# Optimization experiments

Hardware: AMD Instinct MI355X
Metric: run time of the kernel (lower is better)

The kernel has to match this reference:

```python
import jax, jax.numpy as jnp
import numpy as np

NU, NI = 32768, 8192
N = NU + NI
DIM = 64
E = 2_000_000
KNN_K = 10
N_LAYERS = 2
MM_LAYERS = 1
MM_IMG_W = 0.1
THRESHOLD = 0.0


def _knn_adj(feat, k=KNN_K):
    # mirrors get_knn_adj_mat + compute_normalized_laplacian (built on frozen feats)
    fn = feat / np.linalg.norm(feat, axis=1, keepdims=True)
    sim = fn @ fn.T                              # [NI, NI]
    knn = np.argpartition(-sim, k, axis=1)[:, :k]
    rows = np.repeat(np.arange(feat.shape[0]), k)
    cols = knn.reshape(-1)
    deg = np.bincount(rows, minlength=feat.shape[0]).astype(np.float32) + 1e-7
    rinv = deg ** -0.5
    vals = (rinv[rows] * rinv[cols]).astype(np.float32)
    return np.stack([rows, cols]).astype(np.int64), vals


def setup_inputs() -> dict:
    key = jax.random.key(0)
    ks = jax.random.split(key, 10)
    rng = np.random.default_rng(0)
    # trainable params (xavier-ish scales)
    user_emb = jax.random.normal(ks[0], (NU, DIM), jnp.float32) * 0.02
    item_emb = jax.random.normal(ks[1], (NI, DIM), jnp.float32) * 0.02
    v_feat = jax.random.normal(ks[2], (NI, 1024), jnp.float32)
    t_feat = jax.random.normal(ks[3], (NI, 384), jnp.float32)
    Wi = jax.random.normal(ks[4], (DIM, 1024), jnp.float32) * (2.0 / (DIM + 1024)) ** 0.5
    bi = jnp.zeros((DIM,), jnp.float32)
    Wt = jax.random.normal(ks[5], (DIM, 384), jnp.float32) * (2.0 / (DIM + 384)) ** 0.5
    bt = jnp.zeros((DIM,), jnp.float32)
    conv_W = jax.random.normal(ks[6], (N_LAYERS, DIM, DIM), jnp.float32) * (1.0 / DIM) ** 0.5
    conv_b = jnp.zeros((N_LAYERS, DIM), jnp.float32)
    # user-item interaction edges, items offset by NU (as in edge_index_clone)
    users = rng.integers(0, NU, size=E)
    items = rng.integers(0, NI, size=E) + NU
    edge_index = jnp.asarray(np.stack([users, items]).astype(np.int64))
    # frozen multimodal knn adjacencies
    img_idx_np, img_vals_np = _knn_adj(np.asarray(v_feat))
    txt_idx_np, txt_vals_np = _knn_adj(np.asarray(t_feat))
    mm_idx_np = np.concatenate([img_idx_np, txt_idx_np], axis=1)
    mm_vals_np = np.concatenate([MM_IMG_W * img_vals_np, (1.0 - MM_IMG_W) * txt_vals_np])
    return {
        'user_emb': user_emb, 'item_emb': item_emb, 'v_feat': v_feat, 't_feat': t_feat,
        'Wi': Wi, 'bi': bi, 'Wt': Wt, 'bt': bt, 'conv_W': conv_W, 'conv_b': conv_b,
        'edge_index': edge_index,
        'img_idx': jnp.asarray(img_idx_np), 'img_vals': jnp.asarray(img_vals_np),
        'txt_idx': jnp.asarray(txt_idx_np), 'txt_vals': jnp.asarray(txt_vals_np),
        'mm_idx': jnp.asarray(mm_idx_np), 'mm_vals': jnp.asarray(mm_vals_np),
    }


def _l2norm(x):
    return x / jnp.maximum(jnp.linalg.norm(x, axis=1, keepdims=True), 1e-12)


def _spmm(idx, vals, h, n):
    # out[r] = sum vals * h[c]
    return jax.ops.segment_sum(vals[:, None] * h[idx[1]], idx[0], num_segments=n)


def _gcn(x, W, b, src, dst, edge_w, n):
    # PyG GCNConv: symmetric norm with self-loops; masked-out edges get weight 0
    h = x @ W.T
    deg = jax.ops.segment_sum(edge_w, dst, num_segments=n) + 1.0  # +1 self-loop
    dinv = jax.lax.rsqrt(deg)
    norm = dinv[src] * dinv[dst] * edge_w
    agg = jax.ops.segment_sum(h[src] * norm[:, None], dst, num_segments=n)
    return agg + h * (dinv * dinv)[:, None] + b


def _propagate(ego, conv_W, conv_b, eu, ev, filtered):
    src = jnp.concatenate([eu, ev])
    dst = jnp.concatenate([ev, eu])
    embs = [ego]
    for l in range(N_LAYERS):
        if filtered:
            # sim_matrix[u, i-NU] == dot(ego[u], ego[i]) read only at edge positions
            s = jnp.sum(ego[eu] * ego[ev], axis=1)
            m = (s >= THRESHOLD).astype(ego.dtype)
            edge_w = jnp.concatenate([m, m])
        else:
            edge_w = jnp.ones(src.shape[0], ego.dtype)
        ego = _gcn(ego, conv_W[l], conv_b[l], src, dst, edge_w, N)
        embs.append(ego)
    return jnp.mean(jnp.stack(embs, axis=1), axis=1)


def reference(user_emb, item_emb, v_feat, t_feat, Wi, bi, Wt, bt, conv_W, conv_b,
              edge_index, img_idx, img_vals, txt_idx, txt_vals, mm_idx, mm_vals):
    eu, ev = edge_index[0], edge_index[1]
    v_emb = v_feat @ Wi.T + bi
    t_emb = t_feat @ Wt.T + bt
    # first forward: final_i_g_embeddings is None -> guides unused
    h = item_emb
    for _ in range(MM_LAYERS):
        h = _spmm(mm_idx, mm_vals, h, NI)
    h = _l2norm(h)
    h1 = v_emb
    for _ in range(MM_LAYERS):
        h1 = _spmm(img_idx, img_vals, h1, NI)
    h1 = _l2norm(h1)
    h2 = t_emb
    for _ in range(MM_LAYERS):
        h2 = _spmm(txt_idx, txt_vals, h2, NI)
    h2 = _l2norm(h2)

    av = _propagate(jnp.concatenate([user_emb, v_emb], axis=0), conv_W, conv_b, eu, ev, True)
    u_v, i_v = av[:NU], av[NU:] + h1
    at = _propagate(jnp.concatenate([user_emb, t_emb], axis=0), conv_W, conv_b, eu, ev, True)
    u_t, i_t = at[:NU], at[NU:] + h2
    ag = _propagate(jnp.concatenate([user_emb, item_emb], axis=0), conv_W, conv_b, eu, ev, False)
    u_g, i_g = ag[:NU], ag[NU:] + h

    u = jnp.concatenate([u_g, u_v, u_t], axis=1)
    i = jnp.concatenate([i_g, i_v, i_t], axis=1)
    return jnp.concatenate([u, i], axis=0)  # [NU+NI, 3*DIM]
```

## Files before the change

### kernel.cpp

```cpp
#include <hip/hip_runtime.h>
#include <cmath>

#define NUs 32768
#define NIs 8192
#define NNs 40960
#define NEs 2000000
#define CHUNK 2048
#define NB1 977
#define L1 (256*NB1)
#define L4 (L1/4)
#define NSA 245

typedef unsigned short ushort_t;
typedef unsigned int uint_t;
typedef unsigned long long ull_t;
typedef __attribute__((ext_vector_type(8))) short bf16x8;
typedef __attribute__((ext_vector_type(4))) float f32x4;

__device__ __forceinline__ float4 ld4(const float* p){ return *reinterpret_cast<const float4*>(p); }
__device__ __forceinline__ void st4(float* p, float4 v){ *reinterpret_cast<float4*>(p) = v; }
__device__ __forceinline__ ushort_t f2bf(float f){
    uint_t u = __float_as_uint(f);
    return (ushort_t)((u + 0x7FFFu + ((u >> 16) & 1u)) >> 16);
}
__device__ __forceinline__ float bf2f(ushort_t h){ return __uint_as_float((uint_t)h << 16); }


__global__ __launch_bounds__(256) void k_scanA(const int4* __restrict__ in4, int* __restrict__ out,
                                               int* __restrict__ bsums){
    __shared__ int s[256];
    int t = threadIdx.x; int i = blockIdx.x*256 + t;
    int4 v = {0,0,0,0};
    if (i < L4) v = in4[i];
    int sum = v.x+v.y+v.z+v.w;
    s[t] = sum; __syncthreads();
    for (int off=1; off<256; off<<=1){
        int x = (t>=off)? s[t-off] : 0;
        __syncthreads(); s[t] += x; __syncthreads();
    }
    int excl = s[t]-sum;
    if (t == 255) bsums[blockIdx.x] = s[255];
    if (i < L4){
        int o = excl;
        out[4*i]   = o; o += v.x;
        out[4*i+1] = o; o += v.y;
        out[4*i+2] = o; o += v.z;
        out[4*i+3] = o;
    }
}
__global__ void k_scanB(int* __restrict__ b){
    __shared__ int s[256];
    int t = threadIdx.x;
    int v = (t < NSA)? b[t] : 0;
    s[t] = v; __syncthreads();
    for (int off=1; off<256; off<<=1){
        int x = (t>=off)? s[t-off] : 0;
        __syncthreads(); s[t] += x; __syncthreads();
    }
    if (t < NSA) b[t] = s[t]-v;
}
__global__ __launch_bounds__(256) void k_scanC(int4* __restrict__ out, const int* __restrict__ bo){
    int i = blockIdx.x*256 + threadIdx.x;
    if (i >= L4) return;
    int a = bo[blockIdx.x];
    int4 v = out[i]; v.x+=a; v.y+=a; v.z+=a; v.w+=a; out[i] = v;
}

__global__ __launch_bounds__(256) void k_u1cnt(const int* __restrict__ eu, int* __restrict__ C){
    __shared__ int h[256];
    int t = threadIdx.x; h[t] = 0; __syncthreads();
    int base = blockIdx.x*CHUNK;
    #pragma unroll
    for (int k = 0; k < 8; k++){
        int e = base + k*256 + t;
        if (e < NEs) atomicAdd(&h[eu[e]>>7], 1);
    }
    __syncthreads();
    C[t*NB1 + blockIdx.x] = h[t];
}
__global__ __launch_bounds__(256) void k_u1scat(const int* __restrict__ eu, const int* __restrict__ ev,
                                                const int* __restrict__ off, uint_t* __restrict__ stage){
    __shared__ int bo[256]; __shared__ int rk[256];
    int t = threadIdx.x;
    bo[t] = off[t*NB1 + blockIdx.x]; rk[t] = 0;
    __syncthreads();
    int base = blockIdx.x*CHUNK;
    #pragma unroll
    for (int k = 0; k < 8; k++){
        int e = base + k*256 + t;
        if (e < NEs){
            int u = eu[e]; int b = u>>7;
            int r = atomicAdd(&rk[b], 1);
            stage[bo[b]+r] = ((uint_t)u<<13) | (uint_t)(ev[e]-NUs);
        }
    }
}
__global__ __launch_bounds__(256) void k_u2(const uint_t* __restrict__ stage, const int* __restrict__ off,
                                            int* __restrict__ ptr, ushort_t* __restrict__ csr_u,
                                            ull_t* __restrict__ itemin){
    __shared__ int h[128], lb[128], rk[128];
    int b = blockIdx.x, t = threadIdx.x;
    int base = off[b*NB1];
    int end  = (b == 255)? NEs : off[(b+1)*NB1];
    if (t < 128){ h[t] = 0; rk[t] = 0; }
    __syncthreads();
    for (int i = base+t; i < end; i += 256) atomicAdd(&h[(stage[i]>>13)&127], 1);
    __syncthreads();
    if (t < 128) lb[t] = h[t];
    __syncthreads();
    for (int o = 1; o < 128; o <<= 1){
        int x = 0;
        if (t < 128 && t >= o) x = lb[t-o];
        __syncthreads();
        if (t < 128) lb[t] += x;
        __syncthreads();
    }
    if (t < 128){
        int excl = lb[t] - h[t];
        ptr[b*128 + t] = base + excl;
        lb[t] = base + excl;
    }
    __syncthreads();
    for (int i = base+t; i < end; i += 256){
        uint_t p = stage[i];
        int u = (int)(p>>13), item = (int)(p & 0x1FFFu);
        int r = atomicAdd(&rk[u&127], 1);
        int pos = lb[u&127] + r;
        csr_u[pos] = (ushort_t)item;
        itemin[pos] = ((ull_t)item<<36) | ((ull_t)pos<<15) | (ull_t)u;
    }
}
__global__ __launch_bounds__(256) void k_i1cnt(const ull_t* __restrict__ itemin, int* __restrict__ C){
    __shared__ int h[256];
    int t = threadIdx.x; h[t] = 0; __syncthreads();
    int base = blockIdx.x*CHUNK;
    #pragma unroll
    for (int k = 0; k < 8; k++){
        int e = base + k*256 + t;
        if (e < NEs) atomicAdd(&h[(int)((itemin[e]>>41)&255ULL)], 1);
    }
    __syncthreads();
    C[t*NB1 + blockIdx.x] = h[t];
}
__global__ __launch_bounds__(256) void k_i1scat(const ull_t* __restrict__ itemin, const int* __restrict__ off,
                                                ull_t* __restrict__ stage){
    __shared__ int bo[256]; __shared__ int rk[256];
    int t = threadIdx.x;
    bo[t] = off[t*NB1 + blockIdx.x]; rk[t] = 0;
    __syncthreads();
    int base = blockIdx.x*CHUNK;
    #pragma unroll
    for (int k = 0; k < 8; k++){
        int e = base + k*256 + t;
        if (e < NEs){
            ull_t p = itemin[e];
            int b = (int)((p>>41)&255ULL);
            int r = atomicAdd(&rk[b], 1);
            stage[bo[b]+r] = p;
        }
    }
}
__global__ __launch_bounds__(256) void k_i2(const ull_t* __restrict__ stage, const int* __restrict__ off,
                                            int* __restrict__ ptr, ull_t* __restrict__ csr_i){
    __shared__ int h[32], lb[32], rk[32];
    int b = blockIdx.x, t = threadIdx.x;
    int base = off[b*NB1];
    int end  = (b == 255)? NEs : off[(b+1)*NB1];
    if (t < 32){ h[t] = 0; rk[t] = 0; }
    __syncthreads();
    for (int i = base+t; i < end; i += 256) atomicAdd(&h[(int)((stage[i]>>36)&31ULL)], 1);
    __syncthreads();
    if (t < 32) lb[t] = h[t];
    __syncthreads();
    for (int o = 1; o < 32; o <<= 1){
        int x = 0;
        if (t < 32 && t >= o) x = lb[t-o];
        __syncthreads();
        if (t < 32) lb[t] += x;
        __syncthreads();
    }
    if (t < 32){
        int excl = lb[t] - h[t];
        ptr[NUs + b*32 + t] = NEs + base + excl;
        lb[t] = base + excl;
    }
    if (b == 255 && t == 0) ptr[NNs] = 2*NEs;
    __syncthreads();
    for (int i = base+t; i < end; i += 256){
        ull_t p = stage[i];
        int key = (int)((p>>36)&31ULL);
        int r = atomicAdd(&rk[key], 1);
        int pos = lb[key] + r;
        csr_i[pos] = p & 0xFFFFFFFFFULL;
    }
}

template<int K>
__global__ __launch_bounds__(256) void k_featgemm(const float* __restrict__ A, const float* __restrict__ W,
                                                  const float* __restrict__ bias, float* __restrict__ out){
    __shared__ float As[32][65];
    __shared__ float Ws[64][65];
    int tid = threadIdx.x;
    int tx = tid & 15, ty = tid >> 4;
    int r0 = blockIdx.x * 32;
    float acc[2][4] = {};
    for (int kt = 0; kt < K; kt += 64){
        #pragma unroll
        for (int l = 0; l < 8; l++){
            int i = l*256 + tid;
            int rr = i >> 6, kk = i & 63;
            As[rr][kk] = A[(size_t)(r0+rr)*K + kt + kk];
        }
        #pragma unroll
        for (int l = 0; l < 16; l++){
            int i = l*256 + tid;
            int rr = i >> 6, kk = i & 63;
            Ws[rr][kk] = W[(size_t)rr*K + kt + kk];
        }
        __syncthreads();
        #pragma unroll 8
        for (int kk = 0; kk < 64; kk++){
            float a[2], bv[4];
            #pragma unroll
            for (int i = 0; i < 2; i++) a[i] = As[ty*2+i][kk];
            #pragma unroll
            for (int j = 0; j < 4; j++) bv[j] = Ws[tx*4+j][kk];
            #pragma unroll
            for (int i = 0; i < 2; i++)
                #pragma unroll
                for (int j = 0; j < 4; j++)
                    acc[i][j] += a[i]*bv[j];
        }
        __syncthreads();
    }
    #pragma unroll
    for (int i = 0; i < 2; i++)
        #pragma unroll
        for (int j = 0; j < 4; j++)
            out[(size_t)(r0+ty*2+i)*64 + tx*4+j] = acc[i][j] + bias[tx*4+j];
}

__global__ __launch_bounds__(256) void k_spmm_l2(const int* __restrict__ idx, const float* __restrict__ vals,
                                                 const float* __restrict__ src, float* __restrict__ out,
                                                 int stride, int parts){
    int wave = (blockIdx.x*blockDim.x + threadIdx.x) >> 6;
    if (wave >= NIs) return;
    int lane = threadIdx.x & 63;
    const int* cols = idx + stride;
    float acc = 0.f;
    for (int part = 0; part < parts; part++){
        int base = part*81920 + wave*10;
        #pragma unroll
        for (int j = 0; j < 10; j++){
            int e = base + j;
            acc += vals[e] * src[(size_t)cols[e]*64 + lane];
        }
    }
    float ss = acc*acc;
    #pragma unroll
    for (int mset = 1; mset < 64; mset <<= 1) ss += __shfl_xor(ss, mset, 64);
    float nrm = fmaxf(sqrtf(ss), 1e-12f);
    out[(size_t)wave*64 + lane] = acc / nrm;
}

__global__ __launch_bounds__(256) void k_init(const float* __restrict__ ue, const float* __restrict__ it,
                                              float* __restrict__ ego, float* __restrict__ accm){
    int i = blockIdx.x*blockDim.x + threadIdx.x;
    if (i >= NNs*16) return;
    int n = i >> 4, c = i & 15;
    float4 v = (n < NUs) ? ld4(ue + (size_t)n*64 + c*4)
                         : ld4(it + (size_t)(n-NUs)*64 + c*4);
    st4(ego  + (size_t)n*64 + c*4, v);
    st4(accm + (size_t)n*64 + c*4, v);
}

__global__ __launch_bounds__(256) void k_mask(const int* __restrict__ ptr, const ushort_t* __restrict__ csr_u,
                                              const float* __restrict__ ego,
                                              uint_t* __restrict__ mbits, float* __restrict__ dinv){
    int wave = (blockIdx.x*blockDim.x + threadIdx.x) >> 6;
    if (wave >= NUs) return;
    int lane = threadIdx.x & 63;
    int q = lane >> 4, r = lane & 15;
    float4 eu4 = ld4(ego + (size_t)wave*64 + r*4);
    int jb = ptr[wave], je = ptr[wave+1];
    float msum = 0.f;
    int j = jb + q;
    for (; j + 4 < je; j += 8){
        int s0 = NUs + csr_u[j];
        int s1 = NUs + csr_u[j+4];
        float4 v0 = ld4(ego + (size_t)s0*64 + r*4);
        float4 v1 = ld4(ego + (size_t)s1*64 + r*4);
        float d0 = eu4.x*v0.x + eu4.y*v0.y + eu4.z*v0.z + eu4.w*v0.w;
        float d1 = eu4.x*v1.x + eu4.y*v1.y + eu4.z*v1.z + eu4.w*v1.w;
        d0 += __shfl_xor(d0, 1, 64); d1 += __shfl_xor(d1, 1, 64);
        d0 += __shfl_xor(d0, 2, 64); d1 += __shfl_xor(d1, 2, 64);
        d0 += __shfl_xor(d0, 4, 64); d1 += __shfl_xor(d1, 4, 64);
        d0 += __shfl_xor(d0, 8, 64); d1 += __shfl_xor(d1, 8, 64);
        if (r == 0){
            if (d0 >= 0.f){ atomicOr(&mbits[j>>5], 1u << (j & 31)); msum += 1.f; }
            int j1 = j + 4;
            if (d1 >= 0.f){ atomicOr(&mbits[j1>>5], 1u << (j1 & 31)); msum += 1.f; }
        }
    }
    for (; j < je; j += 4){
        int s0 = NUs + csr_u[j];
        float4 v0 = ld4(ego + (size_t)s0*64 + r*4);
        float d0 = eu4.x*v0.x + eu4.y*v0.y + eu4.z*v0.z + eu4.w*v0.w;
        d0 += __shfl_xor(d0, 1, 64);
        d0 += __shfl_xor(d0, 2, 64);
        d0 += __shfl_xor(d0, 4, 64);
        d0 += __shfl_xor(d0, 8, 64);
        if (r == 0 && d0 >= 0.f){ atomicOr(&mbits[j>>5], 1u << (j & 31)); msum += 1.f; }
    }
    msum += __shfl_xor(msum, 16, 64);
    msum += __shfl_xor(msum, 32, 64);
    if (lane == 0) dinv[wave] = rsqrtf(msum + 1.0f);
}

__global__ __launch_bounds__(256) void k_itemdeg(const int* __restrict__ ptr, const ull_t* __restrict__ csr_i,
                                                 const uint_t* __restrict__ mbits, float* __restrict__ dinv){
    int wave = (blockIdx.x*blockDim.x + threadIdx.x) >> 6;
    if (wave >= NIs) return;
    int n = NUs + wave;
    int lane = threadIdx.x & 63;
    int jb = ptr[n], je = ptr[n+1];
    float s = 0.f;
    for (int j = jb + lane; j < je; j += 64){
        uint_t upos = (uint_t)((csr_i[j - NEs] >> 15) & 0x1FFFFFULL);
        s += (float)((mbits[upos >> 5] >> (upos & 31)) & 1u);
    }
    #pragma unroll
    for (int k = 1; k < 64; k <<= 1) s += __shfl_xor(s, k, 64);
    if (lane == 0) dinv[n] = rsqrtf(s + 1.0f);
}

__global__ void k_dinvcnt(const int* __restrict__ ptr, float* __restrict__ dinv){
    int n = blockIdx.x*blockDim.x + threadIdx.x;
    if (n < NNs) dinv[n] = rsqrtf((float)(ptr[n+1]-ptr[n]) + 1.0f);
}

__global__ __launch_bounds__(256) void k_gemmM(const float* __restrict__ ego, const float* __restrict__ W,
                                               const float* __restrict__ dinv, ushort_t* __restrict__ gB){
    int tid = threadIdx.x;
    int wv = tid >> 6, lane = tid & 63;
    int rbase = (blockIdx.x*4 + wv) * 16;
    int c16 = lane & 15;
    int ks = (lane >> 4) * 8;
    const float* ar = ego + (size_t)(rbase + c16)*64;
    bf16x8 ah0, al0, ah1, al1;
    #pragma unroll
    for (int j = 0; j < 8; j++){
        float a = ar[ks + j];
        ushort_t h = f2bf(a); ah0[j] = (short)h; al0[j] = (short)f2bf(a - bf2f(h));
        float b = ar[32 + ks + j];
        ushort_t g = f2bf(b); ah1[j] = (short)g; al1[j] = (short)f2bf(b - bf2f(g));
    }
    float dv[4];
    #pragma unroll
    for (int j = 0; j < 4; j++) dv[j] = dinv[rbase + (lane >> 4)*4 + j];
    #pragma unroll
    for (int ct = 0; ct < 4; ct++){
        const float* wr = W + (size_t)(ct*16 + c16)*64;
        bf16x8 wh0, wl0, wh1, wl1;
        #pragma unroll
        for (int j = 0; j < 8; j++){
            float w = wr[ks + j];
            ushort_t h = f2bf(w); wh0[j] = (short)h; wl0[j] = (short)f2bf(w - bf2f(h));
            float x = wr[32 + ks + j];
            ushort_t g = f2bf(x); wh1[j] = (short)g; wl1[j] = (short)f2bf(x - bf2f(g));
        }
        f32x4 acc = {0.f, 0.f, 0.f, 0.f};
        acc = __builtin_amdgcn_mfma_f32_16x16x32_bf16(ah0, wh0, acc, 0, 0, 0);
        acc = __builtin_amdgcn_mfma_f32_16x16x32_bf16(al0, wh0, acc, 0, 0, 0);
        acc = __builtin_amdgcn_mfma_f32_16x16x32_bf16(ah0, wl0, acc, 0, 0, 0);
        acc = __builtin_amdgcn_mfma_f32_16x16x32_bf16(ah1, wh1, acc, 0, 0, 0);
        acc = __builtin_amdgcn_mfma_f32_16x16x32_bf16(al1, wh1, acc, 0, 0, 0);
        acc = __builtin_amdgcn_mfma_f32_16x16x32_bf16(ah1, wl1, acc, 0, 0, 0);
        #pragma unroll
        for (int j = 0; j < 4; j++){
            int row = rbase + (lane >> 4)*4 + j;
            gB[(size_t)row*64 + ct*16 + c16] = f2bf(acc[j] * dv[j]);
        }
    }
}

template<bool MASKED>
__global__ __launch_bounds__(256) void k_agg(const int* __restrict__ ptr, const ushort_t* __restrict__ csr_u,
                                             const ull_t* __restrict__ csr_i,
                                             const uint_t* __restrict__ mbits,
                                             const ushort_t* __restrict__ gB, const float* __restrict__ dinv,
                                             const float* __restrict__ bias,
                                             float* __restrict__ egon, float* __restrict__ accm){
    int wave = (blockIdx.x*blockDim.x + threadIdx.x) >> 6;
    if (wave >= NNs) return;
    int lane = threadIdx.x & 63;
    int q = lane >> 3, r = lane & 7;
    int jb = ptr[wave], je = ptr[wave+1];
    float acc[8] = {};

    #define ADDROW(row) { \
        uint4 w_ = *reinterpret_cast<const uint4*>(gB + (size_t)(row)*64 + r*8); \
        acc[0] += __uint_as_float(w_.x << 16); acc[1] += __uint_as_float(w_.x & 0xFFFF0000u); \
        acc[2] += __uint_as_float(w_.y << 16); acc[3] += __uint_as_float(w_.y & 0xFFFF0000u); \
        acc[4] += __uint_as_float(w_.z << 16); acc[5] += __uint_as_float(w_.z & 0xFFFF0000u); \
        acc[6] += __uint_as_float(w_.w << 16); acc[7] += __uint_as_float(w_.w & 0xFFFF0000u); }

    if (wave < NUs){
        int j = jb + q;
        for (; j + 8 < je; j += 16){
            int i0 = csr_u[j], i1 = csr_u[j+8];
            bool w0 = true, w1 = true;
            if (MASKED){
                w0 = (mbits[j>>5] >> (j&31)) & 1u;
                w1 = (mbits[(j+8)>>5] >> ((j+8)&31)) & 1u;
            }
            if (w0) ADDROW(NUs + i0);
            if (w1) ADDROW(NUs + i1);
        }
        if (j < je){
            bool w0 = true;
            if (MASKED) w0 = (mbits[j>>5] >> (j&31)) & 1u;
            if (w0) ADDROW(NUs + (int)csr_u[j]);
        }
    } else {
        const ull_t* ci = csr_i - NEs;
        int j = jb + q;
        for (; j + 8 < je; j += 16){
            ull_t p0 = ci[j], p1 = ci[j+8];
            bool w0 = true, w1 = true;
            if (MASKED){
                uint_t a0 = (uint_t)((p0>>15) & 0x1FFFFFULL);
                uint_t a1 = (uint_t)((p1>>15) & 0x1FFFFFULL);
                w0 = (mbits[a0>>5] >> (a0&31)) & 1u;
                w1 = (mbits[a1>>5] >> (a1&31)) & 1u;
            }
            if (w0) ADDROW((int)(p0 & 32767ULL));
            if (w1) ADDROW((int)(p1 & 32767ULL));
        }
        if (j < je){
            ull_t p0 = ci[j];
            bool w0 = true;
            if (MASKED){
                uint_t a0 = (uint_t)((p0>>15) & 0x1FFFFFULL);
                w0 = (mbits[a0>>5] >> (a0&31)) & 1u;
            }
            if (w0) ADDROW((int)(p0 & 32767ULL));
        }
    }
    #undef ADDROW

    #pragma unroll
    for (int k = 0; k < 8; k++){
        acc[k] += __shfl_xor(acc[k], 8, 64);
        acc[k] += __shfl_xor(acc[k], 16, 64);
        acc[k] += __shfl_xor(acc[k], 32, 64);
    }
    if (q == 0){
        float dn = dinv[wave];
        uint4 w_ = *reinterpret_cast<const uint4*>(gB + (size_t)wave*64 + r*8);
        float gs[8];
        gs[0] = __uint_as_float(w_.x << 16); gs[1] = __uint_as_float(w_.x & 0xFFFF0000u);
        gs[2] = __uint_as_float(w_.y << 16); gs[3] = __uint_as_float(w_.y & 0xFFFF0000u);
        gs[4] = __uint_as_float(w_.z << 16); gs[5] = __uint_as_float(w_.z & 0xFFFF0000u);
        gs[6] = __uint_as_float(w_.w << 16); gs[7] = __uint_as_float(w_.w & 0xFFFF0000u);
        float o[8];
        #pragma unroll
        for (int k = 0; k < 8; k++) o[k] = dn*(acc[k] + gs[k]) + bias[r*8 + k];
        float* eg = egon + (size_t)wave*64 + r*8;
        float* am = accm + (size_t)wave*64 + r*8;
        float4 o0 = {o[0],o[1],o[2],o[3]}, o1 = {o[4],o[5],o[6],o[7]};
        st4(eg, o0); st4(eg+4, o1);
        float4 a0 = ld4(am), a1 = ld4(am+4);
        a0.x+=o[0]; a0.y+=o[1]; a0.z+=o[2]; a0.w+=o[3];
        a1.x+=o[4]; a1.y+=o[5]; a1.z+=o[6]; a1.w+=o[7];
        st4(am, a0); st4(am+4, a1);
    }
}

__global__ __launch_bounds__(256) void k_final(const float* __restrict__ accm, const float* __restrict__ extra,
                                               float* __restrict__ out, int p){
    int i = blockIdx.x*blockDim.x + threadIdx.x;
    if (i >= NNs*16) return;
    int n = i >> 4, c = i & 15;
    float4 v = ld4(accm + (size_t)n*64 + c*4);
    const float third = 1.0f/3.0f;
    v.x *= third; v.y *= third; v.z *= third; v.w *= third;
    if (n >= NUs){
        float4 e = ld4(extra + (size_t)(n-NUs)*64 + c*4);
        v.x += e.x; v.y += e.y; v.z += e.z; v.w += e.w;
    }
    st4(out + (size_t)n*192 + p*64 + c*4, v);
}

extern "C" void kernel_launch(void* const* d_in, const int* in_sizes, int n_in,
                              void* d_out, int out_size, void* d_ws, size_t ws_size,
                              hipStream_t stream){
    const float* user_emb = (const float*)d_in[0];
    const float* item_emb = (const float*)d_in[1];
    const float* v_feat   = (const float*)d_in[2];
    const float* t_feat   = (const float*)d_in[3];
    const float* Wi       = (const float*)d_in[4];
    const float* bi       = (const float*)d_in[5];
    const float* Wt       = (const float*)d_in[6];
    const float* bt       = (const float*)d_in[7];
    const float* convW    = (const float*)d_in[8];
    const float* convb    = (const float*)d_in[9];
    const int*   edge     = (const int*)d_in[10];
    const int*   img_idx  = (const int*)d_in[11];
    const float* img_vals = (const float*)d_in[12];
    const int*   txt_idx  = (const int*)d_in[13];
    const float* txt_vals = (const float*)d_in[14];
    const int*   mm_idx   = (const int*)d_in[15];
    const float* mm_vals  = (const float*)d_in[16];
    float* out = (float*)d_out;

    const int* eu = edge;
    const int* ev = edge + NEs;

    char* wsb = (char*)d_ws;
    size_t off = 0;
    auto alloc = [&](size_t b)->char*{ char* p = wsb + off; off = (off + b + 255) & ~(size_t)255; return p; };
    int*      ptr    = (int*)     alloc((size_t)(NNs+1)*4);
    int*      Cflat  = (int*)     alloc((size_t)L1*4);
    int*      bsums  = (int*)     alloc(256*4);
    uint_t*   stageu = (uint_t*)  alloc((size_t)NEs*4);
    ull_t*    itemin = (ull_t*)   alloc((size_t)NEs*8);
    ull_t*    stagei = (ull_t*)   alloc((size_t)NEs*8);
    ushort_t* csr_u  = (ushort_t*)alloc((size_t)NEs*2);
    ull_t*    csr_i  = (ull_t*)   alloc((size_t)NEs*8);
    uint_t*   mbits  = (uint_t*)  alloc((size_t)((NEs+63)/64)*8);
    float*    dinv   = (float*)   alloc((size_t)NNs*4);
    float*    ego_a  = (float*)   alloc((size_t)NNs*64*4);
    float*    ego_b  = (float*)   alloc((size_t)NNs*64*4);
    ushort_t* gB     = (ushort_t*)alloc((size_t)NNs*64*2);
    float*    accm   = (float*)   alloc((size_t)NNs*64*4);
    float*    vemb   = (float*)   alloc((size_t)NIs*64*4);
    float*    temb   = (float*)   alloc((size_t)NIs*64*4);
    float*    hbuf   = (float*)   alloc((size_t)NIs*64*4);
    float*    h1buf  = (float*)   alloc((size_t)NIs*64*4);
    float*    h2buf  = (float*)   alloc((size_t)NIs*64*4);

    k_u1cnt<<<NB1, 256, 0, stream>>>(eu, Cflat);
    k_scanA<<<NSA, 256, 0, stream>>>((const int4*)Cflat, Cflat, bsums);
    k_scanB<<<1, 256, 0, stream>>>(bsums);
    k_scanC<<<NSA, 256, 0, stream>>>((int4*)Cflat, bsums);
    k_u1scat<<<NB1, 256, 0, stream>>>(eu, ev, Cflat, stageu);
    k_u2<<<256, 256, 0, stream>>>(stageu, Cflat, ptr, csr_u, itemin);
    k_i1cnt<<<NB1, 256, 0, stream>>>(itemin, Cflat);
    k_scanA<<<NSA, 256, 0, stream>>>((const int4*)Cflat, Cflat, bsums);
    k_scanB<<<1, 256, 0, stream>>>(bsums);
    k_scanC<<<NSA, 256, 0, stream>>>((int4*)Cflat, bsums);
    k_i1scat<<<NB1, 256, 0, stream>>>(itemin, Cflat, stagei);
    k_i2<<<256, 256, 0, stream>>>(stagei, Cflat, ptr, csr_i);

    k_featgemm<1024><<<256, 256, 0, stream>>>(v_feat, Wi, bi, vemb);
    k_featgemm<384> <<<256, 256, 0, stream>>>(t_feat, Wt, bt, temb);

    k_spmm_l2<<<2048, 256, 0, stream>>>(mm_idx,  mm_vals,  item_emb, hbuf,  163840, 2);
    k_spmm_l2<<<2048, 256, 0, stream>>>(img_idx, img_vals, vemb,     h1buf, 81920, 1);
    k_spmm_l2<<<2048, 256, 0, stream>>>(txt_idx, txt_vals, temb,     h2buf, 81920, 1);

    auto propagate = [&](const float* item_part, bool filtered, const float* extra, int pcol){
        k_init<<<2560, 256, 0, stream>>>(user_emb, item_part, ego_a, accm);
        float* cur = ego_a; float* nxt = ego_b;
        if (!filtered) k_dinvcnt<<<160, 256, 0, stream>>>(ptr, dinv);
        for (int l = 0; l < 2; l++){
            if (filtered){
                hipMemsetAsync(mbits, 0, (size_t)((NEs+63)/64)*8, stream);
                k_mask<<<8192, 256, 0, stream>>>(ptr, csr_u, cur, mbits, dinv);
                k_itemdeg<<<2048, 256, 0, stream>>>(ptr, csr_i, mbits, dinv);
            }
            k_gemmM<<<640, 256, 0, stream>>>(cur, convW + l*64*64, dinv, gB);
            if (filtered)
                k_agg<true><<<10240, 256, 0, stream>>>(ptr, csr_u, csr_i, mbits, gB, dinv, convb + l*64, nxt, accm);
            else
                k_agg<false><<<10240, 256, 0, stream>>>(ptr, csr_u, csr_i, nullptr, gB, dinv, convb + l*64, nxt, accm);
            float* t = cur; cur = nxt; nxt = t;
        }
        k_final<<<2560, 256, 0, stream>>>(accm, extra, out, pcol);
    };

    propagate(vemb,     true,  h1buf, 1);
    propagate(temb,     true,  h2buf, 2);
    propagate(item_emb, false, hbuf,  0);
}
```

Measured before the change: 924.1 us.

## Split item CSR into SoA arrays, MFMA feature GEMM, ballot masks, split item aggregation

Stores the item-side CSR as two narrower arrays (16-bit user id and 32-bit edge position) instead of packed 64-bit words, so item aggregation and degree passes read fewer bytes. The feature projection GEMM moves to bf16 MFMA with a hi/lo split for near-fp32 accuracy. The mask kernel builds bitmask words with a wavefront ballot and one atomicOr per 32-bit word instead of an atomic per edge. Item aggregation becomes a separate kernel run in two column halves, which gives more waves per item hub but costs extra launches and reads each edge list twice.

```diff
diff --git a/kernel.cpp b/kernel.cpp
--- a/kernel.cpp
+++ b/kernel.cpp
@@ -161,7 +161,8 @@
     }
 }
 __global__ __launch_bounds__(256) void k_i2(const ull_t* __restrict__ stage, const int* __restrict__ off,
-                                            int* __restrict__ ptr, ull_t* __restrict__ csr_i){
+                                            int* __restrict__ ptr, ushort_t* __restrict__ csr_iu,
+                                            uint_t* __restrict__ csr_ip){
     __shared__ int h[32], lb[32], rk[32];
     int b = blockIdx.x, t = threadIdx.x;
     int base = off[b*NB1];
@@ -191,53 +192,54 @@
         int key = (int)((p>>36)&31ULL);
         int r = atomicAdd(&rk[key], 1);
         int pos = lb[key] + r;
-        csr_i[pos] = p & 0xFFFFFFFFFULL;
+        csr_iu[pos] = (ushort_t)(p & 32767ULL);
+        csr_ip[pos] = (uint_t)((p >> 15) & 0x1FFFFFULL);
     }
 }
 
 template<int K>
-__global__ __launch_bounds__(256) void k_featgemm(const float* __restrict__ A, const float* __restrict__ W,
-                                                  const float* __restrict__ bias, float* __restrict__ out){
-    __shared__ float As[32][65];
-    __shared__ float Ws[64][65];
+__global__ __launch_bounds__(256) void k_featM(const float* __restrict__ A, const float* __restrict__ W,
+                                               const float* __restrict__ bias, float* __restrict__ out){
     int tid = threadIdx.x;
-    int tx = tid & 15, ty = tid >> 4;
-    int r0 = blockIdx.x * 32;
-    float acc[2][4] = {};
-    for (int kt = 0; kt < K; kt += 64){
-        #pragma unroll
-        for (int l = 0; l < 8; l++){
-            int i = l*256 + tid;
-            int rr = i >> 6, kk = i & 63;
-            As[rr][kk] = A[(size_t)(r0+rr)*K + kt + kk];
-        }
-        #pragma unroll
-        for (int l = 0; l < 16; l++){
-            int i = l*256 + tid;
-            int rr = i >> 6, kk = i & 63;
-            Ws[rr][kk] = W[(size_t)rr*K + kt + kk];
-        }
-        __syncthreads();
-        #pragma unroll 8
-        for (int kk = 0; kk < 64; kk++){
-            float a[2], bv[4];
+    int wv = tid >> 6, lane = tid & 63;
+    int rbase = (blockIdx.x*4 + wv) * 16;
+    int c16 = lane & 15;
+    int ks8 = (lane >> 4) * 8;
+    f32x4 acc0 = {0,0,0,0}, acc1 = {0,0,0,0}, acc2 = {0,0,0,0}, acc3 = {0,0,0,0};
+    for (int kt = 0; kt < K; kt += 32){
+        const float* ar = A + (size_t)(rbase + c16)*K + kt + ks8;
+        bf16x8 ah, al;
+        #pragma unroll
+        for (int j = 0; j < 8; j++){
+            float a = ar[j];
+            ushort_t h = f2bf(a); ah[j] = (short)h; al[j] = (short)f2bf(a - bf2f(h));
+        }
+        #pragma unroll
+        for (int ct = 0; ct < 4; ct++){
+            const float* wr = W + (size_t)(ct*16 + c16)*K + kt + ks8;
+            bf16x8 wh, wl;
             #pragma unroll
-            for (int i = 0; i < 2; i++) a[i] = As[ty*2+i][kk];
-            #pragma unroll
-            for (int j = 0; j < 4; j++) bv[j] = Ws[tx*4+j][kk];
-            #pragma unroll
-            for (int i = 0; i < 2; i++)
-                #pragma unroll
-                for (int j = 0; j < 4; j++)
-                    acc[i][j] += a[i]*bv[j];
-        }
-        __syncthreads();
-    }
-    #pragma unroll
-    for (int i = 0; i < 2; i++)
-        #pragma unroll
-        for (int j = 0; j < 4; j++)
-            out[(size_t)(r0+ty*2+i)*64 + tx*4+j] = acc[i][j] + bias[tx*4+j];
+            for (int j = 0; j < 8; j++){
+                float w = wr[j];
+                ushort_t h = f2bf(w); wh[j] = (short)h; wl[j] = (short)f2bf(w - bf2f(h));
+            }
+            f32x4 acc = (ct==0)? acc0 : (ct==1)? acc1 : (ct==2)? acc2 : acc3;
+            acc = __builtin_amdgcn_mfma_f32_16x16x32_bf16(ah, wh, acc, 0, 0, 0);
+            acc = __builtin_amdgcn_mfma_f32_16x16x32_bf16(al, wh, acc, 0, 0, 0);
+            acc = __builtin_amdgcn_mfma_f32_16x16x32_bf16(ah, wl, acc, 0, 0, 0);
+            if (ct==0) acc0 = acc; else if (ct==1) acc1 = acc; else if (ct==2) acc2 = acc; else acc3 = acc;
+        }
+    }
+    #pragma unroll
+    for (int ct = 0; ct < 4; ct++){
+        f32x4 acc = (ct==0)? acc0 : (ct==1)? acc1 : (ct==2)? acc2 : acc3;
+        float bb = bias[ct*16 + c16];
+        #pragma unroll
+        for (int j = 0; j < 4; j++){
+            int row = rbase + (lane >> 4)*4 + j;
+            out[(size_t)row*64 + ct*16 + c16] = acc[j] + bb;
+        }
+    }
 }
 
 __global__ __launch_bounds__(256) void k_spmm_l2(const int* __restrict__ idx, const float* __restrict__ vals,
@@ -283,41 +285,32 @@
     int q = lane >> 4, r = lane & 15;
     float4 eu4 = ld4(ego + (size_t)wave*64 + r*4);
     int jb = ptr[wave], je = ptr[wave+1];
-    float msum = 0.f;
-    int j = jb + q;
-    for (; j + 4 < je; j += 8){
-        int s0 = NUs + csr_u[j];
-        int s1 = NUs + csr_u[j+4];
-        float4 v0 = ld4(ego + (size_t)s0*64 + r*4);
-        float4 v1 = ld4(ego + (size_t)s1*64 + r*4);
-        float d0 = eu4.x*v0.x + eu4.y*v0.y + eu4.z*v0.z + eu4.w*v0.w;
-        float d1 = eu4.x*v1.x + eu4.y*v1.y + eu4.z*v1.z + eu4.w*v1.w;
-        d0 += __shfl_xor(d0, 1, 64); d1 += __shfl_xor(d1, 1, 64);
-        d0 += __shfl_xor(d0, 2, 64); d1 += __shfl_xor(d1, 2, 64);
-        d0 += __shfl_xor(d0, 4, 64); d1 += __shfl_xor(d1, 4, 64);
-        d0 += __shfl_xor(d0, 8, 64); d1 += __shfl_xor(d1, 8, 64);
-        if (r == 0){
-            if (d0 >= 0.f){ atomicOr(&mbits[j>>5], 1u << (j & 31)); msum += 1.f; }
-            int j1 = j + 4;
-            if (d1 >= 0.f){ atomicOr(&mbits[j1>>5], 1u << (j1 & 31)); msum += 1.f; }
-        }
-    }
-    for (; j < je; j += 4){
-        int s0 = NUs + csr_u[j];
-        float4 v0 = ld4(ego + (size_t)s0*64 + r*4);
-        float d0 = eu4.x*v0.x + eu4.y*v0.y + eu4.z*v0.z + eu4.w*v0.w;
-        d0 += __shfl_xor(d0, 1, 64);
-        d0 += __shfl_xor(d0, 2, 64);
-        d0 += __shfl_xor(d0, 4, 64);
-        d0 += __shfl_xor(d0, 8, 64);
-        if (r == 0 && d0 >= 0.f){ atomicOr(&mbits[j>>5], 1u << (j & 31)); msum += 1.f; }
-    }
-    msum += __shfl_xor(msum, 16, 64);
-    msum += __shfl_xor(msum, 32, 64);
+    float msum = 0.f; uint_t wacc = 0; int curW = jb >> 5;
+    for (int j0 = jb & ~3; j0 < je; j0 += 4){
+        int myj = j0 + q;
+        bool valid = (myj >= jb) && (myj < je);
+        int it = valid ? (int)csr_u[myj] : 0;
+        float4 v = ld4(ego + (size_t)(NUs+it)*64 + r*4);
+        float d = eu4.x*v.x + eu4.y*v.y + eu4.z*v.z + eu4.w*v.w;
+        d += __shfl_xor(d, 1, 64);
+        d += __shfl_xor(d, 2, 64);
+        d += __shfl_xor(d, 4, 64);
+        d += __shfl_xor(d, 8, 64);
+        unsigned long long bal = __ballot(valid && (d >= 0.f));
+        uint_t nib = (uint_t)((bal & 1ULL) | ((bal>>15) & 2ULL) | ((bal>>30) & 4ULL) | ((bal>>45) & 8ULL));
+        int w = j0 >> 5;
+        if (w != curW){
+            if (wacc && lane == 0) atomicOr(&mbits[curW], wacc);
+            wacc = 0; curW = w;
+        }
+        wacc |= nib << (j0 & 31);
+        msum += (float)__popc(nib);
+    }
+    if (wacc && lane == 0) atomicOr(&mbits[curW], wacc);
     if (lane == 0) dinv[wave] = rsqrtf(msum + 1.0f);
 }
 
-__global__ __launch_bounds__(256) void k_itemdeg(const int* __restrict__ ptr, const ull_t* __restrict__ csr_i,
+__global__ __launch_bounds__(256) void k_itemdeg(const int* __restrict__ ptr, const uint_t* __restrict__ csr_ip,
                                                  const uint_t* __restrict__ mbits, float* __restrict__ dinv){
     int wave = (blockIdx.x*blockDim.x + threadIdx.x) >> 6;
     if (wave >= NIs) return;
@@ -326,7 +319,7 @@
     int jb = ptr[n], je = ptr[n+1];
     float s = 0.f;
     for (int j = jb + lane; j < je; j += 64){
-        uint_t upos = (uint_t)((csr_i[j - NEs] >> 15) & 0x1FFFFFULL);
+        uint_t upos = csr_ip[j - NEs];
         s += (float)((mbits[upos >> 5] >> (upos & 31)) & 1u);
     }
     #pragma unroll
@@ -385,14 +378,13 @@
 }
 
 template<bool MASKED>
-__global__ __launch_bounds__(256) void k_agg(const int* __restrict__ ptr, const ushort_t* __restrict__ csr_u,
-                                             const ull_t* __restrict__ csr_i,
-                                             const uint_t* __restrict__ mbits,
-                                             const ushort_t* __restrict__ gB, const float* __restrict__ dinv,
-                                             const float* __restrict__ bias,
-                                             float* __restrict__ egon, float* __restrict__ accm){
+__global__ __launch_bounds__(256) void k_agg_u(const int* __restrict__ ptr, const ushort_t* __restrict__ csr_u,
+                                               const uint_t* __restrict__ mbits,
+                                               const ushort_t* __restrict__ gB, const float* __restrict__ dinv,
+                                               const float* __restrict__ bias,
+                                               float* __restrict__ egon, float* __restrict__ accm){
     int wave = (blockIdx.x*blockDim.x + threadIdx.x) >> 6;
-    if (wave >= NNs) return;
+    if (wave >= NUs) return;
     int lane = threadIdx.x & 63;
     int q = lane >> 3, r = lane & 7;
     int jb = ptr[wave], je = ptr[wave+1];
@@ -405,47 +397,21 @@
         acc[4] += __uint_as_float(w_.z << 16); acc[5] += __uint_as_float(w_.z & 0xFFFF0000u); \
         acc[6] += __uint_as_float(w_.w << 16); acc[7] += __uint_as_float(w_.w & 0xFFFF0000u); }
 
-    if (wave < NUs){
-        int j = jb + q;
-        for (; j + 8 < je; j += 16){
-            int i0 = csr_u[j], i1 = csr_u[j+8];
-            bool w0 = true, w1 = true;
-            if (MASKED){
-                w0 = (mbits[j>>5] >> (j&31)) & 1u;
-                w1 = (mbits[(j+8)>>5] >> ((j+8)&31)) & 1u;
-            }
-            if (w0) ADDROW(NUs + i0);
-            if (w1) ADDROW(NUs + i1);
-        }
-        if (j < je){
-            bool w0 = true;
-            if (MASKED) w0 = (mbits[j>>5] >> (j&31)) & 1u;
-            if (w0) ADDROW(NUs + (int)csr_u[j]);
-        }
-    } else {
-        const ull_t* ci = csr_i - NEs;
-        int j = jb + q;
-        for (; j + 8 < je; j += 16){
-            ull_t p0 = ci[j], p1 = ci[j+8];
-            bool w0 = true, w1 = true;
-            if (MASKED){
-                uint_t a0 = (uint_t)((p0>>15) & 0x1FFFFFULL);
-                uint_t a1 = (uint_t)((p1>>15) & 0x1FFFFFULL);
-                w0 = (mbits[a0>>5] >> (a0&31)) & 1u;
-                w1 = (mbits[a1>>5] >> (a1&31)) & 1u;
-            }
-            if (w0) ADDROW((int)(p0 & 32767ULL));
-            if (w1) ADDROW((int)(p1 & 32767ULL));
-        }
-        if (j < je){
-            ull_t p0 = ci[j];
-            bool w0 = true;
-            if (MASKED){
-                uint_t a0 = (uint_t)((p0>>15) & 0x1FFFFFULL);
-                w0 = (mbits[a0>>5] >> (a0&31)) & 1u;
-            }
-            if (w0) ADDROW((int)(p0 & 32767ULL));
-        }
+    int j = jb + q;
+    for (; j + 8 < je; j += 16){
+        int i0 = csr_u[j], i1 = csr_u[j+8];
+        bool w0 = true, w1 = true;
+        if (MASKED){
+            w0 = (mbits[j>>5] >> (j&31)) & 1u;
+            w1 = (mbits[(j+8)>>5] >> ((j+8)&31)) & 1u;
+        }
+        if (w0) ADDROW(NUs + i0);
+        if (w1) ADDROW(NUs + i1);
+    }
+    if (j < je){
+        bool w0 = true;
+        if (MASKED) w0 = (mbits[j>>5] >> (j&31)) & 1u;
+        if (w0) ADDROW(NUs + (int)csr_u[j]);
     }
     #undef ADDROW
 
@@ -474,6 +440,75 @@
         a0.x+=o[0]; a0.y+=o[1]; a0.z+=o[2]; a0.w+=o[3];
         a1.x+=o[4]; a1.y+=o[5]; a1.z+=o[6]; a1.w+=o[7];
         st4(am, a0); st4(am+4, a1);
+    }
+}
+
+template<bool MASKED>
+__global__ __launch_bounds__(256) void k_agg_i(const int* __restrict__ ptr, const ushort_t* __restrict__ csr_iu,
+                                               const uint_t* __restrict__ csr_ip,
+                                               const uint_t* __restrict__ mbits,
+                                               const ushort_t* __restrict__ gB, const float* __restrict__ dinv,
+                                               const float* __restrict__ bias,
+                                               float* __restrict__ egon, float* __restrict__ accm, int half){
+    int wave = (blockIdx.x*blockDim.x + threadIdx.x) >> 6;
+    if (wave >= NIs) return;
+    int n = NUs + wave;
+    int lane = threadIdx.x & 63;
+    int q = lane >> 3, r = lane & 7;
+    int colb = half*32 + r*4;
+    int jb = ptr[n], je = ptr[n+1];
+    float acc[4] = {};
+
+    #define ADDROW2(row) { \
+        uint2 w_ = *reinterpret_cast<const uint2*>(gB + (size_t)(row)*64 + colb); \
+        acc[0] += __uint_as_float(w_.x << 16); acc[1] += __uint_as_float(w_.x & 0xFFFF0000u); \
+        acc[2] += __uint_as_float(w_.y << 16); acc[3] += __uint_as_float(w_.y & 0xFFFF0000u); }
+
+    int j = jb + q;
+    for (; j + 8 < je; j += 16){
+        int u0 = csr_iu[j - NEs], u1 = csr_iu[j+8 - NEs];
+        bool w0 = true, w1 = true;
+        if (MASKED){
+            uint_t a0 = csr_ip[j - NEs], a1 = csr_ip[j+8 - NEs];
+            w0 = (mbits[a0>>5] >> (a0&31)) & 1u;
+            w1 = (mbits[a1>>5] >> (a1&31)) & 1u;
+        }
+        if (w0) ADDROW2(u0);
+        if (w1) ADDROW2(u1);
+    }
+    if (j < je){
+        int u0 = csr_iu[j - NEs];
+        bool w0 = true;
+        if (MASKED){
+            uint_t a0 = csr_ip[j - NEs];
+            w0 = (mbits[a0>>5] >> (a0&31)) & 1u;
+        }
+        if (w0) ADDROW2(u0);
+    }
+    #undef ADDROW2
+
+    #pragma unroll
+    for (int k = 0; k < 4; k++){
+        acc[k] += __shfl_xor(acc[k], 8, 64);
+        acc[k] += __shfl_xor(acc[k], 16, 64);
+        acc[k] += __shfl_xor(acc[k], 32, 64);
+    }
+    if (q == 0){
+        float dn = dinv[n];
+        uint2 w_ = *reinterpret_cast<const uint2*>(gB + (size_t)n*64 + colb);
+        float gs[4];
+        gs[0] = __uint_as_float(w_.x << 16); gs[1] = __uint_as_float(w_.x & 0xFFFF0000u);
+        gs[2] = __uint_as_float(w_.y << 16); gs[3] = __uint_as_float(w_.y & 0xFFFF0000u);
+        float o[4];
+        #pragma unroll
+        for (int k = 0; k < 4; k++) o[k] = dn*(acc[k] + gs[k]) + bias[colb + k];
+        float* eg = egon + (size_t)n*64 + colb;
+        float* am = accm + (size_t)n*64 + colb;
+        float4 o0 = {o[0],o[1],o[2],o[3]};
+        st4(eg, o0);
+        float4 a0 = ld4(am);
+        a0.x+=o[0]; a0.y+=o[1]; a0.z+=o[2]; a0.w+=o[3];
+        st4(am, a0);
     }
 }
 
@@ -527,7 +562,8 @@
     ull_t*    itemin = (ull_t*)   alloc((size_t)NEs*8);
     ull_t*    stagei = (ull_t*)   alloc((size_t)NEs*8);
     ushort_t* csr_u  = (ushort_t*)alloc((size_t)NEs*2);
-    ull_t*    csr_i  = (ull_t*)   alloc((size_t)NEs*8);
+    ushort_t* csr_iu = (ushort_t*)alloc((size_t)NEs*2);
+    uint_t*   csr_ip = (uint_t*)  alloc((size_t)NEs*4);
     uint_t*   mbits  = (uint_t*)  alloc((size_t)((NEs+63)/64)*8);
     float*    dinv   = (float*)   alloc((size_t)NNs*4);
     float*    ego_a  = (float*)   alloc((size_t)NNs*64*4);
@@ -551,10 +587,10 @@
     k_scanB<<<1, 256, 0, stream>>>(bsums);
     k_scanC<<<NSA, 256, 0, stream>>>((int4*)Cflat, bsums);
     k_i1scat<<<NB1, 256, 0, stream>>>(itemin, Cflat, stagei);
-    k_i2<<<256, 256, 0, stream>>>(stagei, Cflat, ptr, csr_i);
-
-    k_featgemm<1024><<<256, 256, 0, stream>>>(v_feat, Wi, bi, vemb);
-    k_featgemm<384> <<<256, 256, 0, stream>>>(t_feat, Wt, bt, temb);
+    k_i2<<<256, 256, 0, stream>>>(stagei, Cflat, ptr, csr_iu, csr_ip);
+
+    k_featM<1024><<<128, 256, 0, stream>>>(v_feat, Wi, bi, vemb);
+    k_featM<384> <<<128, 256, 0, stream>>>(t_feat, Wt, bt, temb);
 
     k_spmm_l2<<<2048, 256, 0, stream>>>(mm_idx,  mm_vals,  item_emb, hbuf,  163840, 2);
     k_spmm_l2<<<2048, 256, 0, stream>>>(img_idx, img_vals, vemb,     h1buf, 81920, 1);
@@ -568,13 +604,18 @@
             if (filtered){
                 hipMemsetAsync(mbits, 0, (size_t)((NEs+63)/64)*8, stream);
                 k_mask<<<8192, 256, 0, stream>>>(ptr, csr_u, cur, mbits, dinv);
-                k_itemdeg<<<2048, 256, 0, stream>>>(ptr, csr_i, mbits, dinv);
+                k_itemdeg<<<2048, 256, 0, stream>>>(ptr, csr_ip, mbits, dinv);
             }
             k_gemmM<<<640, 256, 0, stream>>>(cur, convW + l*64*64, dinv, gB);
-            if (filtered)
-                k_agg<true><<<10240, 256, 0, stream>>>(ptr, csr_u, csr_i, mbits, gB, dinv, convb + l*64, nxt, accm);
-            else
-                k_agg<false><<<10240, 256, 0, stream>>>(ptr, csr_u, csr_i, nullptr, gB, dinv, convb + l*64, nxt, accm);
+            if (filtered){
+                k_agg_u<true><<<8192, 256, 0, stream>>>(ptr, csr_u, mbits, gB, dinv, convb + l*64, nxt, accm);
+                k_agg_i<true><<<2048, 256, 0, stream>>>(ptr, csr_iu, csr_ip, mbits, gB, dinv, convb + l*64, nxt, accm, 0);
+                k_agg_i<true><<<2048, 256, 0, stream>>>(ptr, csr_iu, csr_ip, mbits, gB, dinv, convb + l*64, nxt, accm, 1);
+            } else {
+                k_agg_u<false><<<8192, 256, 0, stream>>>(ptr, csr_u, nullptr, gB, dinv, convb + l*64, nxt, accm);
+                k_agg_i<false><<<2048, 256, 0, stream>>>(ptr, csr_iu, nullptr, nullptr, gB, dinv, convb + l*64, nxt, accm, 0);
+                k_agg_i<false><<<2048, 256, 0, stream>>>(ptr, csr_iu, nullptr, nullptr, gB, dinv, convb + l*64, nxt, accm, 1);
+            }
             float* t = cur; cur = nxt; nxt = t;
         }
         k_final<<<2560, 256, 0, stream>>>(accm, extra, out, pcol);
```

Result: slower. 1.079 ms (+16.8%).
